# Kernel optimization log

Measured on AMD Instinct MI355X. Metric: run time of the kernel, lower is better.

The kernel has to match this reference:

```python
import jax, jax.numpy as jnp
import numpy as np

N = 50000      # nodes
E = 800000     # edges (includes N self-loops)
IN = 256       # input feature dim
HID = 64       # hidden per head
H = 4          # heads (all layers)
C = 40         # num classes
SLOPE = 0.2    # leaky relu negative slope


def setup_inputs() -> dict:
    key = jax.random.key(0)
    ks = jax.random.split(key, 20)
    Er = E - N
    src = jnp.concatenate([jax.random.randint(ks[0], (Er,), 0, N), jnp.arange(N)]).astype(jnp.int32)
    dst = jnp.concatenate([jax.random.randint(ks[1], (Er,), 0, N), jnp.arange(N)]).astype(jnp.int32)

    def w(k, shape, fan):
        return jax.random.normal(k, shape, jnp.float32) * (1.0 / np.sqrt(fan))

    return {
        "x": jax.random.normal(ks[2], (N, IN), jnp.float32),
        "src": src, "dst": dst,
        # layer 0: IN -> H*HID, no residual, elu
        "W0": w(ks[3], (IN, H * HID), IN),
        "al0": w(ks[4], (H, HID), HID), "ar0": w(ks[5], (H, HID), HID),
        "b0": jnp.zeros((H, HID), jnp.float32),
        # layer 1: H*HID -> H*HID, identity residual, elu
        "W1": w(ks[6], (H * HID, H * HID), H * HID),
        "al1": w(ks[7], (H, HID), HID), "ar1": w(ks[8], (H, HID), HID),
        "b1": jnp.zeros((H, HID), jnp.float32),
        # output layer: H*HID -> H*C, linear residual, no activation
        "W2": w(ks[9], (H * HID, H * C), H * HID),
        "al2": w(ks[10], (H, C), C), "ar2": w(ks[11], (H, C), C),
        "b2": jnp.zeros((H, C), jnp.float32),
        "Wres2": w(ks[12], (H * HID, H * C), H * HID),
    }


def _gat_conv(x, src, dst, W, al, ar, b, res, act):
    """One DGL-style GATConv. x: (N, Fin); returns (N, H, D)."""
    h, d = al.shape
    feat = (x @ W).reshape(-1, h, d)                      # (N,H,D)
    el = jnp.einsum("nhd,hd->nh", feat, al)               # (N,H)
    er = jnp.einsum("nhd,hd->nh", feat, ar)               # (N,H)
    e = jax.nn.leaky_relu(el[src] + er[dst], SLOPE)       # (E,H)
    # segment softmax over incoming edges of each destination node
    m = jax.ops.segment_max(e, dst, num_segments=N)       # (N,H)
    ex = jnp.exp(e - m[dst])                              # (E,H)
    denom = jax.ops.segment_sum(ex, dst, num_segments=N)  # (N,H)
    alpha = ex / denom[dst]                               # (E,H)
    out = jax.ops.segment_sum(feat[src] * alpha[:, :, None], dst, num_segments=N)
    if res is not None:
        out = out + res
    out = out + b
    return act(out) if act is not None else out


def reference(x, src, dst, W0, al0, ar0, b0, W1, al1, ar1, b1, W2, al2, ar2, b2, Wres2):
    elu = jax.nn.elu
    h = _gat_conv(x, src, dst, W0, al0, ar0, b0, None, elu).reshape(N, H * HID)
    res1 = h.reshape(N, H, HID)  # identity residual (dims match)
    h = _gat_conv(h, src, dst, W1, al1, ar1, b1, res1, elu).reshape(N, H * HID)
    res2 = (h @ Wres2).reshape(N, H, C)
    out = _gat_conv(h, src, dst, W2, al2, ar2, b2, res2, None)  # (N,H,C)
    return out.mean(axis=1)  # (N,C)
```

## Files before the change

kernel.cpp:

```cpp
#include <hip/hip_runtime.h>
#include <hip/hip_bf16.h>
#include <hip/hip_fp16.h>

#define N_NODES 50000
#define N_EDGES 800000
#define DIN 256
#define HID 64
#define NH 4
#define NC 40

typedef __attribute__((ext_vector_type(4))) short short4v;
typedef __attribute__((ext_vector_type(8))) short bf16x8;
typedef __attribute__((ext_vector_type(4))) float f32x4;

__device__ __forceinline__ unsigned short f2bf(float f) {
    unsigned u = __float_as_uint(f);
    unsigned r = (u + 0x7fffu + ((u >> 16) & 1u)) >> 16;
    return (unsigned short)r;
}
__device__ __forceinline__ float bf2f(unsigned short b) {
    return __uint_as_float(((unsigned)b) << 16);
}


__global__ void k_hist(const int* __restrict__ dst, int* __restrict__ cnt, int E) {
    int i = blockIdx.x * blockDim.x + threadIdx.x;
    if (i < E) atomicAdd(&cnt[dst[i]], 1);
}

#define SCAN_BLOCKS 49

__global__ __launch_bounds__(256) void k_bsum(const int* __restrict__ cnt,
                                              int* __restrict__ bsum, int Nn) {
    __shared__ int red[256];
    int b = blockIdx.x, t = threadIdx.x;
    int base = b * 1024 + t * 4;
    int s = 0;
    if (base + 3 < Nn) {
        int4 v = *(const int4*)(cnt + base);
        s = v.x + v.y + v.z + v.w;
    } else {
        for (int j = 0; j < 4; ++j)
            if (base + j < Nn) s += cnt[base + j];
    }
    red[t] = s;
    __syncthreads();
    for (int off = 128; off; off >>= 1) {
        if (t < off) red[t] += red[t + off];
        __syncthreads();
    }
    if (t == 0) bsum[b] = red[0];
}

__global__ void k_bscan(const int* __restrict__ bsum, int* __restrict__ bpre, int nb) {
    int l = threadIdx.x;
    int x = (l < nb) ? bsum[l] : 0;
    int v = x;
    for (int off = 1; off < 64; off <<= 1) {
        int u = __shfl_up(v, off);
        if (l >= off) v += u;
    }
    if (l < nb) bpre[l] = v - x;
}

__global__ __launch_bounds__(256) void k_scatter(const int* __restrict__ cnt,
                                                 const int* __restrict__ bpre,
                                                 int* __restrict__ rowptr,
                                                 int* __restrict__ cursor, int Nn) {
    __shared__ int red[256];
    int b = blockIdx.x, t = threadIdx.x;
    int base = b * 1024 + t * 4;
    int c[4];
    int s = 0;
    for (int j = 0; j < 4; ++j) {
        int idx = base + j;
        c[j] = (idx < Nn) ? cnt[idx] : 0;
        s += c[j];
    }
    red[t] = s;
    __syncthreads();
    for (int off = 1; off < 256; off <<= 1) {
        int v = (t >= off) ? red[t - off] : 0;
        __syncthreads();
        red[t] += v;
        __syncthreads();
    }
    int run = red[t] - s + bpre[b];
    for (int j = 0; j < 4; ++j) {
        int idx = base + j;
        if (idx < Nn) {
            rowptr[idx] = run;
            cursor[idx] = run;
            run += c[j];
        }
    }
    if (b == 0 && t == 0) rowptr[Nn] = N_EDGES;
}

__global__ void k_fill(const int* __restrict__ src, const int* __restrict__ dst,
                       int* __restrict__ cursor, int* __restrict__ col, int E) {
    int i = blockIdx.x * blockDim.x + threadIdx.x;
    if (i < E) {
        int p = atomicAdd(&cursor[dst[i]], 1);
        col[p] = src[i];
    }
}


__global__ void cvt_wT(const float* __restrict__ W, short* __restrict__ hT,
                       short* __restrict__ lT, int K, int NN) {
    int t = blockIdx.x * blockDim.x + threadIdx.x;
    if (t >= K * NN) return;
    int n = t / K, k = t - n * K;
    float v = W[(size_t)k * NN + n];
    unsigned short h = f2bf(v);
    hT[t] = (short)h;
    lT[t] = (short)f2bf(v - bf2f(h));
}

__global__ void cvt_wT_cat(const float* __restrict__ W2, const float* __restrict__ Wr,
                           short* __restrict__ hT, short* __restrict__ lT) {
    int t = blockIdx.x * blockDim.x + threadIdx.x;
    if (t >= 320 * 256) return;
    int n = t >> 8, k = t & 255;
    float v = (n < 160) ? W2[(size_t)k * 160 + n] : Wr[(size_t)k * 160 + (n - 160)];
    unsigned short h = f2bf(v);
    hT[t] = (short)h;
    lT[t] = (short)f2bf(v - bf2f(h));
}


#define SK 40

__global__ __launch_bounds__(256) void gemm_mfma(const float* __restrict__ A,
                                                 const short* __restrict__ BhT,
                                                 const short* __restrict__ BlT,
                                                 __half* __restrict__ C,
                                                 int M, int NN, int K) {
    __shared__ short Ah[128 * SK], Al[128 * SK], Bh[128 * SK], Bl[128 * SK];
    const int tid = threadIdx.x;
    const int bm = blockIdx.y * 128;
    const int bn = blockIdx.x * 128;
    const int w = tid >> 6, l = tid & 63;
    const int wr = w >> 1, wc = w & 1;
    const int rowf = l & 15, kg = l >> 4;

    f32x4 acc[4][4] = {};

    for (int k0 = 0; k0 < K; k0 += 32) {
        __syncthreads();
#pragma unroll
        for (int it = 0; it < 4; ++it) {
            int chunk = tid + it * 256;
            int row = chunk >> 3, kc = chunk & 7;
            f32x4 v = {};
            int ar = bm + row;
            if (ar < M) v = *(const f32x4*)(A + (size_t)ar * K + k0 + kc * 4);
            short4v hi, lo;
#pragma unroll
            for (int j = 0; j < 4; ++j) {
                unsigned short h_ = f2bf(v[j]);
                hi[j] = (short)h_;
                lo[j] = (short)f2bf(v[j] - bf2f(h_));
            }
            *(short4v*)&Ah[row * SK + kc * 4] = hi;
            *(short4v*)&Al[row * SK + kc * 4] = lo;
        }
#pragma unroll
        for (int it = 0; it < 4; ++it) {
            int chunk = tid + it * 256;
            int tile = chunk >> 9, c2 = chunk & 511;
            int nrow = c2 >> 2, kc = c2 & 3;
            bf16x8 v = {};
            int gn = bn + nrow;
            const short* srcT = tile ? BlT : BhT;
            if (gn < NN) v = *(const bf16x8*)(srcT + (size_t)gn * K + k0 + kc * 8);
            short* dstT = tile ? Bl : Bh;
            *(bf16x8*)&dstT[nrow * SK + kc * 8] = v;
        }
        __syncthreads();

        bf16x8 afh[4], afl[4], bfh[4], bfl[4];
#pragma unroll
        for (int m = 0; m < 4; ++m) {
            int off = (wr * 64 + m * 16 + rowf) * SK + kg * 8;
            afh[m] = *(const bf16x8*)&Ah[off];
            afl[m] = *(const bf16x8*)&Al[off];
        }
#pragma unroll
        for (int n = 0; n < 4; ++n) {
            int off = (wc * 64 + n * 16 + rowf) * SK + kg * 8;
            bfh[n] = *(const bf16x8*)&Bh[off];
            bfl[n] = *(const bf16x8*)&Bl[off];
        }
#pragma unroll
        for (int m = 0; m < 4; ++m)
#pragma unroll
            for (int n = 0; n < 4; ++n) {
                acc[m][n] = __builtin_amdgcn_mfma_f32_16x16x32_bf16(afh[m], bfh[n], acc[m][n], 0, 0, 0);
                acc[m][n] = __builtin_amdgcn_mfma_f32_16x16x32_bf16(afh[m], bfl[n], acc[m][n], 0, 0, 0);
                acc[m][n] = __builtin_amdgcn_mfma_f32_16x16x32_bf16(afl[m], bfh[n], acc[m][n], 0, 0, 0);
            }
    }

#pragma unroll
    for (int m = 0; m < 4; ++m)
#pragma unroll
        for (int r = 0; r < 4; ++r) {
            int grow = bm + wr * 64 + m * 16 + kg * 4 + r;
            if (grow >= M) continue;
#pragma unroll
            for (int n = 0; n < 4; ++n) {
                int gcol = bn + wc * 64 + n * 16 + rowf;
                if (gcol < NN) C[(size_t)grow * NN + gcol] = __float2half(acc[m][n][r]);
            }
        }
}

__global__ __launch_bounds__(256) void elr64(const __half* __restrict__ feat,
                                             const float* __restrict__ al,
                                             const float* __restrict__ ar,
                                             float* __restrict__ el,
                                             float* __restrict__ er, int Nn) {
    int wave = threadIdx.x >> 6, lane = threadIdx.x & 63;
    int n = blockIdx.x * 4 + wave;
    if (n >= Nn) return;
    int g = lane >> 4;
    int i4 = (lane & 15) * 4;
    int off = g * 64 + i4;
    uint2 u = *(const uint2*)(feat + (size_t)n * 256 + off);
    float4 a4 = *(const float4*)(al + off);
    float4 r4 = *(const float4*)(ar + off);
    float2 lo = __half22float2(*(const __half2*)&u.x);
    float2 hi = __half22float2(*(const __half2*)&u.y);
    float sl = lo.x * a4.x + lo.y * a4.y + hi.x * a4.z + hi.y * a4.w;
    float sr = lo.x * r4.x + lo.y * r4.y + hi.x * r4.z + hi.y * r4.w;
#pragma unroll
    for (int o = 8; o; o >>= 1) {
        sl += __shfl_down(sl, o);
        sr += __shfl_down(sr, o);
    }
    if ((lane & 15) == 0) {
        el[n * 4 + g] = sl;
        er[n * 4 + g] = sr;
    }
}

__global__ void elr_gen(const __half* __restrict__ feat, int ld,
                        const float* __restrict__ al, const float* __restrict__ ar,
                        float* __restrict__ el, float* __restrict__ er, int Nn, int D) {
    int i = blockIdx.x * blockDim.x + threadIdx.x;
    if (i >= Nn * NH) return;
    int n = i / NH, h = i % NH;
    const __half* f = feat + (size_t)n * ld + h * D;
    const float* a = al + h * D;
    const float* r = ar + h * D;
    float sl = 0.f, sr = 0.f;
#pragma unroll
    for (int q = 0; q < 10; ++q) {
        uint2 u = *(const uint2*)(f + q * 4);
        float2 lo = __half22float2(*(const __half2*)&u.x);
        float2 hi = __half22float2(*(const __half2*)&u.y);
        sl += lo.x * a[q * 4] + lo.y * a[q * 4 + 1] + hi.x * a[q * 4 + 2] + hi.y * a[q * 4 + 3];
        sr += lo.x * r[q * 4] + lo.y * r[q * 4 + 1] + hi.x * r[q * 4 + 2] + hi.y * r[q * 4 + 3];
    }
    el[i] = sl;
    er[i] = sr;
}

__global__ __launch_bounds__(256) void gat_agg64(const __half* __restrict__ feat,
                                                 const float* __restrict__ el,
                                                 const float* __restrict__ er,
                                                 const int* __restrict__ rowptr,
                                                 const int* __restrict__ col,
                                                 const float* __restrict__ bias,
                                                 const float* __restrict__ res,
                                                 float* __restrict__ out) {
    int wave = threadIdx.x >> 6, lane = threadIdx.x & 63;
    int n = blockIdx.x * 4 + wave;
    if (n >= N_NODES) return;
    int h = lane >> 4;
    int f0 = lane * 4;
    int r0 = rowptr[n], r1 = rowptr[n + 1];
    float ern = er[n * 4 + h];

    float m = -1e30f, denom = 0.f;
    float4 acc = make_float4(0.f, 0.f, 0.f, 0.f);

    float e0 = 0.f, e1 = 0.f, e2 = 0.f, e3 = 0.f;
    uint2 u0 = {0, 0}, u1 = {0, 0}, u2 = {0, 0}, u3 = {0, 0};
    int kl = r0;
    if (kl < r1) { int s = col[kl]; e0 = el[s * 4 + h]; u0 = *(const uint2*)(feat + (size_t)s * 256 + f0); ++kl; }
    if (kl < r1) { int s = col[kl]; e1 = el[s * 4 + h]; u1 = *(const uint2*)(feat + (size_t)s * 256 + f0); ++kl; }
    if (kl < r1) { int s = col[kl]; e2 = el[s * 4 + h]; u2 = *(const uint2*)(feat + (size_t)s * 256 + f0); ++kl; }
    if (kl < r1) { int s = col[kl]; e3 = el[s * 4 + h]; u3 = *(const uint2*)(feat + (size_t)s * 256 + f0); ++kl; }

    for (int k = r0; k < r1; ++k) {
        float e = e0 + ern;
        e = e > 0.f ? e : 0.2f * e;
        float mn = fmaxf(m, e);
        float scale = __expf(m - mn);
        float p = __expf(e - mn);
        m = mn;
        float2 flo = __half22float2(*(const __half2*)&u0.x);
        float2 fhi = __half22float2(*(const __half2*)&u0.y);
        denom = denom * scale + p;
        acc.x = acc.x * scale + p * flo.x;
        acc.y = acc.y * scale + p * flo.y;
        acc.z = acc.z * scale + p * fhi.x;
        acc.w = acc.w * scale + p * fhi.y;
        e0 = e1; u0 = u1;
        e1 = e2; u1 = u2;
        e2 = e3; u2 = u3;
        if (kl < r1) { int s = col[kl]; e3 = el[s * 4 + h]; u3 = *(const uint2*)(feat + (size_t)s * 256 + f0); ++kl; }
    }
    float inv = 1.f / denom;
    float4 b4 = *(const float4*)(bias + f0);
    float4 o = make_float4(acc.x * inv + b4.x, acc.y * inv + b4.y,
                           acc.z * inv + b4.z, acc.w * inv + b4.w);
    if (res) {
        float4 rv = *(const float4*)(res + (size_t)n * 256 + f0);
        o.x += rv.x; o.y += rv.y; o.z += rv.z; o.w += rv.w;
    }
    o.x = o.x > 0.f ? o.x : __expf(o.x) - 1.f;
    o.y = o.y > 0.f ? o.y : __expf(o.y) - 1.f;
    o.z = o.z > 0.f ? o.z : __expf(o.z) - 1.f;
    o.w = o.w > 0.f ? o.w : __expf(o.w) - 1.f;
    *(float4*)(out + (size_t)n * 256 + f0) = o;
}

__global__ __launch_bounds__(256) void gat_agg40(const __half* __restrict__ feat, int ld,
                                                 const float* __restrict__ el,
                                                 const float* __restrict__ er,
                                                 const int* __restrict__ rowptr,
                                                 const int* __restrict__ col,
                                                 const float* __restrict__ bias,
                                                 const __half* __restrict__ res,
                                                 float* __restrict__ out) {
    int wave = threadIdx.x >> 6, lane = threadIdx.x & 63;
    int n = blockIdx.x * 4 + wave;
    if (n >= N_NODES) return;
    float4 o = make_float4(0.f, 0.f, 0.f, 0.f);
    if (lane < 40) {
        int h = lane / 10;
        int f0 = lane * 4;
        int r0 = rowptr[n], r1 = rowptr[n + 1];
        float ern = er[n * 4 + h];
        float m = -1e30f, denom = 0.f;
        float4 acc = make_float4(0.f, 0.f, 0.f, 0.f);

        float e0 = 0.f, e1 = 0.f, e2 = 0.f, e3 = 0.f;
        uint2 u0 = {0, 0}, u1 = {0, 0}, u2 = {0, 0}, u3 = {0, 0};
        int kl = r0;
        if (kl < r1) { int s = col[kl]; e0 = el[s * 4 + h]; u0 = *(const uint2*)(feat + (size_t)s * ld + f0); ++kl; }
        if (kl < r1) { int s = col[kl]; e1 = el[s * 4 + h]; u1 = *(const uint2*)(feat + (size_t)s * ld + f0); ++kl; }
        if (kl < r1) { int s = col[kl]; e2 = el[s * 4 + h]; u2 = *(const uint2*)(feat + (size_t)s * ld + f0); ++kl; }
        if (kl < r1) { int s = col[kl]; e3 = el[s * 4 + h]; u3 = *(const uint2*)(feat + (size_t)s * ld + f0); ++kl; }

        for (int k = r0; k < r1; ++k) {
            float e = e0 + ern;
            e = e > 0.f ? e : 0.2f * e;
            float mn = fmaxf(m, e);
            float scale = __expf(m - mn);
            float p = __expf(e - mn);
            m = mn;
            float2 flo = __half22float2(*(const __half2*)&u0.x);
            float2 fhi = __half22float2(*(const __half2*)&u0.y);
            denom = denom * scale + p;
            acc.x = acc.x * scale + p * flo.x;
            acc.y = acc.y * scale + p * flo.y;
            acc.z = acc.z * scale + p * fhi.x;
            acc.w = acc.w * scale + p * fhi.y;
            e0 = e1; u0 = u1;
            e1 = e2; u1 = u2;
            e2 = e3; u2 = u3;
            if (kl < r1) { int s = col[kl]; e3 = el[s * 4 + h]; u3 = *(const uint2*)(feat + (size_t)s * ld + f0); ++kl; }
        }
        float inv = 1.f / denom;
        float4 b4 = *(const float4*)(bias + f0);
        uint2 ur = *(const uint2*)(res + (size_t)n * ld + f0);
        float2 rlo = __half22float2(*(const __half2*)&ur.x);
        float2 rhi = __half22float2(*(const __half2*)&ur.y);
        o = make_float4(acc.x * inv + b4.x + rlo.x, acc.y * inv + b4.y + rlo.y,
                        acc.z * inv + b4.z + rhi.x, acc.w * inv + b4.w + rhi.y);
    }
    float4 t;
    t.x = o.x + __shfl_down(o.x, 10) + __shfl_down(o.x, 20) + __shfl_down(o.x, 30);
    t.y = o.y + __shfl_down(o.y, 10) + __shfl_down(o.y, 20) + __shfl_down(o.y, 30);
    t.z = o.z + __shfl_down(o.z, 10) + __shfl_down(o.z, 20) + __shfl_down(o.z, 30);
    t.w = o.w + __shfl_down(o.w, 10) + __shfl_down(o.w, 20) + __shfl_down(o.w, 30);
    if (lane < 10) {
        float4 r4 = make_float4(0.25f * t.x, 0.25f * t.y, 0.25f * t.z, 0.25f * t.w);
        *(float4*)(out + (size_t)n * 40 + lane * 4) = r4;
    }
}


extern "C" void kernel_launch(void* const* d_in, const int* in_sizes, int n_in,
                              void* d_out, int out_size, void* d_ws, size_t ws_size,
                              hipStream_t stream) {
    const float* x    = (const float*)d_in[0];
    const int* src    = (const int*)d_in[1];
    const int* dst    = (const int*)d_in[2];
    const float* W0   = (const float*)d_in[3];
    const float* al0  = (const float*)d_in[4];
    const float* ar0  = (const float*)d_in[5];
    const float* b0   = (const float*)d_in[6];
    const float* W1   = (const float*)d_in[7];
    const float* al1  = (const float*)d_in[8];
    const float* ar1  = (const float*)d_in[9];
    const float* b1   = (const float*)d_in[10];
    const float* W2   = (const float*)d_in[11];
    const float* al2  = (const float*)d_in[12];
    const float* ar2  = (const float*)d_in[13];
    const float* b2   = (const float*)d_in[14];
    const float* Wres2 = (const float*)d_in[15];
    float* out = (float*)d_out;

    char* ws = (char*)d_ws;
    auto alloc = [&](size_t bytes) {
        char* p = ws;
        ws += (bytes + 255) & ~(size_t)255;
        return p;
    };
    int* rowptr   = (int*)alloc((N_NODES + 1) * sizeof(int));
    int* cursor   = (int*)alloc(N_NODES * sizeof(int));
    int* cnt      = (int*)alloc(N_NODES * sizeof(int));
    int* bsum     = (int*)alloc(SCAN_BLOCKS * sizeof(int));
    int* bpre     = (int*)alloc(SCAN_BLOCKS * sizeof(int));
    int* colA     = (int*)alloc(N_EDGES * sizeof(int));
    float* el     = (float*)alloc((size_t)N_NODES * NH * sizeof(float));
    float* er     = (float*)alloc((size_t)N_NODES * NH * sizeof(float));
    float* bufB   = (float*)alloc((size_t)N_NODES * 256 * sizeof(float));
    float* bufC   = (float*)alloc((size_t)N_NODES * 256 * sizeof(float));
    __half* featH = (__half*)alloc((size_t)N_NODES * 256 * sizeof(__half));
    __half* featH2= (__half*)alloc((size_t)N_NODES * 320 * sizeof(__half));
    short* W0hT   = (short*)alloc(256 * 256 * sizeof(short));
    short* W0lT   = (short*)alloc(256 * 256 * sizeof(short));
    short* W1hT   = (short*)alloc(256 * 256 * sizeof(short));
    short* W1lT   = (short*)alloc(256 * 256 * sizeof(short));
    short* WchT   = (short*)alloc(320 * 256 * sizeof(short));
    short* WclT   = (short*)alloc(320 * 256 * sizeof(short));

    hipMemsetAsync(cnt, 0, N_NODES * sizeof(int), stream);
    k_hist<<<(N_EDGES + 255) / 256, 256, 0, stream>>>(dst, cnt, N_EDGES);
    k_bsum<<<SCAN_BLOCKS, 256, 0, stream>>>(cnt, bsum, N_NODES);
    k_bscan<<<1, 64, 0, stream>>>(bsum, bpre, SCAN_BLOCKS);
    k_scatter<<<SCAN_BLOCKS, 256, 0, stream>>>(cnt, bpre, rowptr, cursor, N_NODES);
    k_fill<<<(N_EDGES + 255) / 256, 256, 0, stream>>>(src, dst, cursor, colA, N_EDGES);

    cvt_wT<<<(256 * 256 + 255) / 256, 256, 0, stream>>>(W0, W0hT, W0lT, 256, 256);
    cvt_wT<<<(256 * 256 + 255) / 256, 256, 0, stream>>>(W1, W1hT, W1lT, 256, 256);
    cvt_wT_cat<<<(320 * 256 + 255) / 256, 256, 0, stream>>>(W2, Wres2, WchT, WclT);

    dim3 g256(2, (N_NODES + 127) / 128);
    dim3 g320(3, (N_NODES + 127) / 128);
    int agg_grid = (N_NODES + 3) / 4;

    gemm_mfma<<<g256, 256, 0, stream>>>(x, W0hT, W0lT, featH, N_NODES, 256, 256);
    elr64<<<(N_NODES + 3) / 4, 256, 0, stream>>>(featH, al0, ar0, el, er, N_NODES);
    gat_agg64<<<agg_grid, 256, 0, stream>>>(featH, el, er, rowptr, colA, b0, nullptr, bufB);

    gemm_mfma<<<g256, 256, 0, stream>>>(bufB, W1hT, W1lT, featH, N_NODES, 256, 256);
    elr64<<<(N_NODES + 3) / 4, 256, 0, stream>>>(featH, al1, ar1, el, er, N_NODES);
    gat_agg64<<<agg_grid, 256, 0, stream>>>(featH, el, er, rowptr, colA, b1, bufB, bufC);

    gemm_mfma<<<g320, 256, 0, stream>>>(bufC, WchT, WclT, featH2, N_NODES, 320, 256);
    elr_gen<<<(N_NODES * NH + 255) / 256, 256, 0, stream>>>(featH2, 320, al2, ar2, el, er, N_NODES, NC);
    gat_agg40<<<agg_grid, 256, 0, stream>>>(featH2, 320, el, er, rowptr, colA, b2, featH2 + 160, out);
}
```

Baseline: 692.5 us.

## Precompute per-node max logit to replace online softmax in aggregation

Adds a k_emax pass that computes, per destination node and head, the max of el over incoming edges. Because leaky-relu is monotonic, max(el)+er passed through leaky-relu gives the exact row max, so the aggregation kernels can drop the online rescaling and its second exp per edge. The edge loops also change from a rolling 4-deep prefetch to batches of 4 independent loads. The cost is one extra kernel launch per layer plus an extra gather of col and el over all edges.

Result: faster. 648.2 us (-6.4%).

```diff
diff --git a/kernel.cpp b/kernel.cpp
--- a/kernel.cpp
+++ b/kernel.cpp
@@ -268,9 +268,28 @@
     er[i] = sr;
 }
 
+__global__ __launch_bounds__(256) void k_emax(const float* __restrict__ el,
+                                              const int* __restrict__ rowptr,
+                                              const int* __restrict__ col,
+                                              float* __restrict__ mx) {
+    int wave = threadIdx.x >> 6, lane = threadIdx.x & 63;
+    int n = blockIdx.x * 4 + wave;
+    if (n >= N_NODES) return;
+    int h = lane >> 4, sub = lane & 15;
+    int r0 = rowptr[n], r1 = rowptr[n + 1];
+    float m = -1e30f;
+    for (int k = r0 + sub; k < r1; k += 16)
+        m = fmaxf(m, el[col[k] * 4 + h]);
+#pragma unroll
+    for (int off = 8; off; off >>= 1)
+        m = fmaxf(m, __shfl_xor(m, off));
+    if (sub == 0) mx[n * 4 + h] = m;
+}
+
 __global__ __launch_bounds__(256) void gat_agg64(const __half* __restrict__ feat,
                                                  const float* __restrict__ el,
                                                  const float* __restrict__ er,
+                                                 const float* __restrict__ mx,
                                                  const int* __restrict__ rowptr,
                                                  const int* __restrict__ col,
                                                  const float* __restrict__ bias,
@@ -283,37 +302,47 @@
     int f0 = lane * 4;
     int r0 = rowptr[n], r1 = rowptr[n + 1];
     float ern = er[n * 4 + h];
-
-    float m = -1e30f, denom = 0.f;
+    float M = mx[n * 4 + h] + ern;
+    M = M > 0.f ? M : 0.2f * M;
+
+    float denom = 0.f;
     float4 acc = make_float4(0.f, 0.f, 0.f, 0.f);
 
-    float e0 = 0.f, e1 = 0.f, e2 = 0.f, e3 = 0.f;
-    uint2 u0 = {0, 0}, u1 = {0, 0}, u2 = {0, 0}, u3 = {0, 0};
-    int kl = r0;
-    if (kl < r1) { int s = col[kl]; e0 = el[s * 4 + h]; u0 = *(const uint2*)(feat + (size_t)s * 256 + f0); ++kl; }
-    if (kl < r1) { int s = col[kl]; e1 = el[s * 4 + h]; u1 = *(const uint2*)(feat + (size_t)s * 256 + f0); ++kl; }
-    if (kl < r1) { int s = col[kl]; e2 = el[s * 4 + h]; u2 = *(const uint2*)(feat + (size_t)s * 256 + f0); ++kl; }
-    if (kl < r1) { int s = col[kl]; e3 = el[s * 4 + h]; u3 = *(const uint2*)(feat + (size_t)s * 256 + f0); ++kl; }
-
-    for (int k = r0; k < r1; ++k) {
-        float e = e0 + ern;
-        e = e > 0.f ? e : 0.2f * e;
-        float mn = fmaxf(m, e);
-        float scale = __expf(m - mn);
-        float p = __expf(e - mn);
-        m = mn;
-        float2 flo = __half22float2(*(const __half2*)&u0.x);
-        float2 fhi = __half22float2(*(const __half2*)&u0.y);
-        denom = denom * scale + p;
-        acc.x = acc.x * scale + p * flo.x;
-        acc.y = acc.y * scale + p * flo.y;
-        acc.z = acc.z * scale + p * fhi.x;
-        acc.w = acc.w * scale + p * fhi.y;
-        e0 = e1; u0 = u1;
-        e1 = e2; u1 = u2;
-        e2 = e3; u2 = u3;
-        if (kl < r1) { int s = col[kl]; e3 = el[s * 4 + h]; u3 = *(const uint2*)(feat + (size_t)s * 256 + f0); ++kl; }
-    }
+#define EDGE64(ev, uv)                                         \
+    {                                                          \
+        float e = (ev) + ern;                                  \
+        e = e > 0.f ? e : 0.2f * e;                            \
+        float p = __expf(e - M);                               \
+        float2 flo = __half22float2(*(const __half2*)&(uv).x); \
+        float2 fhi = __half22float2(*(const __half2*)&(uv).y); \
+        denom += p;                                            \
+        acc.x += p * flo.x;                                    \
+        acc.y += p * flo.y;                                    \
+        acc.z += p * fhi.x;                                    \
+        acc.w += p * fhi.y;                                    \
+    }
+
+    int k = r0;
+    for (; k + 4 <= r1; k += 4) {
+        int s0 = col[k], s1 = col[k + 1], s2 = col[k + 2], s3 = col[k + 3];
+        float ea = el[s0 * 4 + h], eb = el[s1 * 4 + h], ec = el[s2 * 4 + h], ed = el[s3 * 4 + h];
+        uint2 ua = *(const uint2*)(feat + (size_t)s0 * 256 + f0);
+        uint2 ub = *(const uint2*)(feat + (size_t)s1 * 256 + f0);
+        uint2 uc = *(const uint2*)(feat + (size_t)s2 * 256 + f0);
+        uint2 ud = *(const uint2*)(feat + (size_t)s3 * 256 + f0);
+        EDGE64(ea, ua);
+        EDGE64(eb, ub);
+        EDGE64(ec, uc);
+        EDGE64(ed, ud);
+    }
+    for (; k < r1; ++k) {
+        int s = col[k];
+        float ev = el[s * 4 + h];
+        uint2 u = *(const uint2*)(feat + (size_t)s * 256 + f0);
+        EDGE64(ev, u);
+    }
+#undef EDGE64
+
     float inv = 1.f / denom;
     float4 b4 = *(const float4*)(bias + f0);
     float4 o = make_float4(acc.x * inv + b4.x, acc.y * inv + b4.y,
@@ -332,6 +361,7 @@
 __global__ __launch_bounds__(256) void gat_agg40(const __half* __restrict__ feat, int ld,
                                                  const float* __restrict__ el,
                                                  const float* __restrict__ er,
+                                                 const float* __restrict__ mx,
                                                  const int* __restrict__ rowptr,
                                                  const int* __restrict__ col,
                                                  const float* __restrict__ bias,
@@ -346,36 +376,46 @@
         int f0 = lane * 4;
         int r0 = rowptr[n], r1 = rowptr[n + 1];
         float ern = er[n * 4 + h];
-        float m = -1e30f, denom = 0.f;
+        float M = mx[n * 4 + h] + ern;
+        M = M > 0.f ? M : 0.2f * M;
+        float denom = 0.f;
         float4 acc = make_float4(0.f, 0.f, 0.f, 0.f);
 
-        float e0 = 0.f, e1 = 0.f, e2 = 0.f, e3 = 0.f;
-        uint2 u0 = {0, 0}, u1 = {0, 0}, u2 = {0, 0}, u3 = {0, 0};
-        int kl = r0;
-        if (kl < r1) { int s = col[kl]; e0 = el[s * 4 + h]; u0 = *(const uint2*)(feat + (size_t)s * ld + f0); ++kl; }
-        if (kl < r1) { int s = col[kl]; e1 = el[s * 4 + h]; u1 = *(const uint2*)(feat + (size_t)s * ld + f0); ++kl; }
-        if (kl < r1) { int s = col[kl]; e2 = el[s * 4 + h]; u2 = *(const uint2*)(feat + (size_t)s * ld + f0); ++kl; }
-        if (kl < r1) { int s = col[kl]; e3 = el[s * 4 + h]; u3 = *(const uint2*)(feat + (size_t)s * ld + f0); ++kl; }
-
-        for (int k = r0; k < r1; ++k) {
-            float e = e0 + ern;
-            e = e > 0.f ? e : 0.2f * e;
-            float mn = fmaxf(m, e);
-            float scale = __expf(m - mn);
-            float p = __expf(e - mn);
-            m = mn;
-            float2 flo = __half22float2(*(const __half2*)&u0.x);
-            float2 fhi = __half22float2(*(const __half2*)&u0.y);
-            denom = denom * scale + p;
-            acc.x = acc.x * scale + p * flo.x;
-            acc.y = acc.y * scale + p * flo.y;
-            acc.z = acc.z * scale + p * fhi.x;
-            acc.w = acc.w * scale + p * fhi.y;
-            e0 = e1; u0 = u1;
-            e1 = e2; u1 = u2;
-            e2 = e3; u2 = u3;
-            if (kl < r1) { int s = col[kl]; e3 = el[s * 4 + h]; u3 = *(const uint2*)(feat + (size_t)s * ld + f0); ++kl; }
-        }
+#define EDGE40(ev, uv)                                         \
+    {                                                          \
+        float e = (ev) + ern;                                  \
+        e = e > 0.f ? e : 0.2f * e;                            \
+        float p = __expf(e - M);                               \
+        float2 flo = __half22float2(*(const __half2*)&(uv).x); \
+        float2 fhi = __half22float2(*(const __half2*)&(uv).y); \
+        denom += p;                                            \
+        acc.x += p * flo.x;                                    \
+        acc.y += p * flo.y;                                    \
+        acc.z += p * fhi.x;                                    \
+        acc.w += p * fhi.y;                                    \
+    }
+
+        int k = r0;
+        for (; k + 4 <= r1; k += 4) {
+            int s0 = col[k], s1 = col[k + 1], s2 = col[k + 2], s3 = col[k + 3];
+            float ea = el[s0 * 4 + h], eb = el[s1 * 4 + h], ec = el[s2 * 4 + h], ed = el[s3 * 4 + h];
+            uint2 ua = *(const uint2*)(feat + (size_t)s0 * ld + f0);
+            uint2 ub = *(const uint2*)(feat + (size_t)s1 * ld + f0);
+            uint2 uc = *(const uint2*)(feat + (size_t)s2 * ld + f0);
+            uint2 ud = *(const uint2*)(feat + (size_t)s3 * ld + f0);
+            EDGE40(ea, ua);
+            EDGE40(eb, ub);
+            EDGE40(ec, uc);
+            EDGE40(ed, ud);
+        }
+        for (; k < r1; ++k) {
+            int s = col[k];
+            float ev = el[s * 4 + h];
+            uint2 u = *(const uint2*)(feat + (size_t)s * ld + f0);
+            EDGE40(ev, u);
+        }
+#undef EDGE40
+
         float inv = 1.f / denom;
         float4 b4 = *(const float4*)(bias + f0);
         uint2 ur = *(const uint2*)(res + (size_t)n * ld + f0);
@@ -431,6 +471,7 @@
     int* colA     = (int*)alloc(N_EDGES * sizeof(int));
     float* el     = (float*)alloc((size_t)N_NODES * NH * sizeof(float));
     float* er     = (float*)alloc((size_t)N_NODES * NH * sizeof(float));
+    float* mx     = (float*)alloc((size_t)N_NODES * NH * sizeof(float));
     float* bufB   = (float*)alloc((size_t)N_NODES * 256 * sizeof(float));
     float* bufC   = (float*)alloc((size_t)N_NODES * 256 * sizeof(float));
     __half* featH = (__half*)alloc((size_t)N_NODES * 256 * sizeof(__half));
@@ -458,14 +499,17 @@
     int agg_grid = (N_NODES + 3) / 4;
 
     gemm_mfma<<<g256, 256, 0, stream>>>(x, W0hT, W0lT, featH, N_NODES, 256, 256);
-    elr64<<<(N_NODES + 3) / 4, 256, 0, stream>>>(featH, al0, ar0, el, er, N_NODES);
-    gat_agg64<<<agg_grid, 256, 0, stream>>>(featH, el, er, rowptr, colA, b0, nullptr, bufB);
+    elr64<<<agg_grid, 256, 0, stream>>>(featH, al0, ar0, el, er, N_NODES);
+    k_emax<<<agg_grid, 256, 0, stream>>>(el, rowptr, colA, mx);
+    gat_agg64<<<agg_grid, 256, 0, stream>>>(featH, el, er, mx, rowptr, colA, b0, nullptr, bufB);
 
     gemm_mfma<<<g256, 256, 0, stream>>>(bufB, W1hT, W1lT, featH, N_NODES, 256, 256);
-    elr64<<<(N_NODES + 3) / 4, 256, 0, stream>>>(featH, al1, ar1, el, er, N_NODES);
-    gat_agg64<<<agg_grid, 256, 0, stream>>>(featH, el, er, rowptr, colA, b1, bufB, bufC);
+    elr64<<<agg_grid, 256, 0, stream>>>(featH, al1, ar1, el, er, N_NODES);
+    k_emax<<<agg_grid, 256, 0, stream>>>(el, rowptr, colA, mx);
+    gat_agg64<<<agg_grid, 256, 0, stream>>>(featH, el, er, mx, rowptr, colA, b1, bufB, bufC);
 
     gemm_mfma<<<g320, 256, 0, stream>>>(bufC, WchT, WclT, featH2, N_NODES, 320, 256);
     elr_gen<<<(N_NODES * NH + 255) / 256, 256, 0, stream>>>(featH2, 320, al2, ar2, el, er, N_NODES, NC);
-    gat_agg40<<<agg_grid, 256, 0, stream>>>(featH2, 320, el, er, rowptr, colA, b2, featH2 + 160, out);
-}
+    k_emax<<<agg_grid, 256, 0, stream>>>(el, rowptr, colA, mx);
+    gat_agg40<<<agg_grid, 256, 0, stream>>>(featH2, 320, el, er, mx, rowptr, colA, b2, featH2 + 160, out);
+}
```
